# Kernel tuning notes

Measured on AMD Instinct MI355X. Metric: run time of the kernel, lower is better.

## Reference

```python
import jax, jax.numpy as jnp
import numpy as np

B, S, D = 2, 2048, 1024
H, K = 16, 64  # num_heads, n_hidden per head


def setup_inputs() -> dict:
    key = jax.random.key(0)
    ks = jax.random.split(key, 10)
    sc = 1.0 / np.sqrt(D)
    x = jax.random.normal(ks[0], (B, S, D), dtype=jnp.float32)
    attn_mask = jax.random.randint(ks[1], (B, S, S), 0, 2, dtype=jnp.int32)
    # per-head nn.Linear(d_input, n_hidden) weights stacked over heads: [H, D, K]
    W_Q = jax.random.normal(ks[2], (H, D, K), dtype=jnp.float32) * sc
    b_Q = jax.random.normal(ks[3], (H, K), dtype=jnp.float32) * sc
    W_K = jax.random.normal(ks[4], (H, D, K), dtype=jnp.float32) * sc
    b_K = jax.random.normal(ks[5], (H, K), dtype=jnp.float32) * sc
    W_V = jax.random.normal(ks[6], (H, D, K), dtype=jnp.float32) * sc
    b_V = jax.random.normal(ks[7], (H, K), dtype=jnp.float32) * sc
    # output projection nn.Linear(H*K, D)
    W_proj = jax.random.normal(ks[8], (H * K, D), dtype=jnp.float32) / np.sqrt(H * K)
    b_proj = jax.random.normal(ks[9], (D,), dtype=jnp.float32) / np.sqrt(H * K)
    return {"x": x, "W_Q": W_Q, "b_Q": b_Q, "W_K": W_K, "b_K": b_K,
            "W_V": W_V, "b_V": b_V, "W_proj": W_proj, "b_proj": b_proj,
            "attn_mask": attn_mask}


def reference(x, W_Q, b_Q, W_K, b_K, W_V, b_V, W_proj, b_proj, attn_mask):
    # Q/K/V for all heads at once: [B, H, S, K]
    Q = jnp.einsum('bsd,hdk->bhsk', x, W_Q) + b_Q[None, :, None, :]
    Kt = jnp.einsum('bsd,hdk->bhsk', x, W_K) + b_K[None, :, None, :]
    V = jnp.einsum('bsd,hdk->bhsk', x, W_V) + b_V[None, :, None, :]
    scale = 1.0 / np.sqrt(K).astype(np.float32)
    scores = jnp.einsum('bhsk,bhtk->bhst', Q, Kt) * scale  # [B,H,S,S]
    neg_inf = jnp.finfo(scores.dtype).min
    scores = jnp.where(attn_mask[:, None, :, :] == 0, neg_inf, scores)
    attn_scores = jax.nn.softmax(scores, axis=-1)  # [B,H,S,S]
    heads = jnp.einsum('bhst,bhtk->bhsk', attn_scores, V)  # [B,H,S,K]
    # concat heads along feature dim -> [B, S, H*K]
    concat = heads.transpose(0, 2, 1, 3).reshape(B, S, H * K)
    attn_output = concat @ W_proj + b_proj  # [B, S, D]
    return attn_output, attn_scores
```

## Files before the change

kernel.cpp:

```cpp
#include <hip/hip_runtime.h>

typedef unsigned short u16;
typedef unsigned long long u64;
typedef __attribute__((ext_vector_type(8))) short short8;
typedef __attribute__((ext_vector_type(8))) float float8;
typedef __attribute__((ext_vector_type(4))) float floatx4;

__device__ __forceinline__ float bf2f(u16 b) { return __uint_as_float(((unsigned)b) << 16); }
__device__ __forceinline__ u16 f2bf(float f) {
    unsigned u = __float_as_uint(f);
    return (u16)((u + 0x7FFFu + ((u >> 16) & 1u)) >> 16);
}

#define MFMA(a, b, c) __builtin_amdgcn_mfma_f32_16x16x32_bf16((a), (b), (c), 0, 0, 0)

#define AST 40
#define KST 72

__global__ __launch_bounds__(256) void k_proj_head(
    const float* __restrict__ x, const float* __restrict__ w, const float* __restrict__ bias,
    u16* __restrict__ out, int mode)
{
    int mt = blockIdx.x, h = blockIdx.y;
    int tid = threadIdx.x, wave = tid >> 6, lane = tid & 63;
    int col = lane & 15, quad = lane >> 4, m0 = wave * 16;
    int rg0 = mt * 64;

    __shared__ u16 As[64 * AST];
    __shared__ u16 Bs[64 * AST];

    floatx4 acc[4];
    for (int i = 0; i < 4; i++) acc[i] = (floatx4){0.f, 0.f, 0.f, 0.f};

    int lr = tid >> 2, lc = (tid & 3) * 8;
    int dr = tid >> 3, nc = (tid & 7) * 8;
    const float* wh = w + (size_t)h * 65536;

    for (int dk = 0; dk < 1024; dk += 32) {
        float8 av = *(const float8*)&x[(size_t)(rg0 + lr) * 1024 + dk + lc];
        short8 a8;
        #pragma unroll
        for (int j = 0; j < 8; j++) a8[j] = (short)f2bf(av[j]);
        *(short8*)&As[lr * AST + lc] = a8;
        float8 wv = *(const float8*)&wh[(size_t)(dk + dr) * 64 + nc];
        #pragma unroll
        for (int j = 0; j < 8; j++) Bs[(nc + j) * AST + dr] = f2bf(wv[j]);
        __syncthreads();
        short8 a = *(const short8*)&As[(m0 + col) * AST + quad * 8];
        #pragma unroll
        for (int nt = 0; nt < 4; nt++) {
            short8 b = *(const short8*)&Bs[(nt * 16 + col) * AST + quad * 8];
            acc[nt] = MFMA(a, b, acc[nt]);
        }
        __syncthreads();
    }
    #pragma unroll
    for (int nt = 0; nt < 4; nt++) {
        int n = nt * 16 + col;
        float bv = bias[h * 64 + n];
        #pragma unroll
        for (int r = 0; r < 4; r++) {
            int rowl = m0 + quad * 4 + r;
            int rg = rg0 + rowl;
            int bb = rg >> 11, s = rg & 2047;
            size_t bh = (size_t)(bb * 16 + h);
            float v = acc[nt][r] + bv;
            if (mode == 0) out[(bh * 2048 + s) * 64 + n] = f2bf(v);
            else           out[(bh * 64 + n) * 2048 + s] = f2bf(v);
        }
    }
}

__global__ __launch_bounds__(256) void k_pack(
    const int* __restrict__ mask, u64* __restrict__ bits)
{
    int row = blockIdx.x;
    int b = row >> 11, s = row & 2047;
    int wv = threadIdx.x >> 6, lane = threadIdx.x & 63;
    for (int w = wv; w < 32; w += 4) {
        int m = mask[(size_t)row * 2048 + w * 64 + lane];
        u64 bal = __ballot(m != 0);
        if (lane == 0) bits[((size_t)(b * 32 + w)) * 2048 + s] = bal;
    }
}

__global__ __launch_bounds__(256, 4) void k_fused(
    const float* __restrict__ x, const float* __restrict__ wq, const float* __restrict__ bq,
    const u16* __restrict__ Kbuf, const u16* __restrict__ Vt,
    const u64* __restrict__ mbits,
    float* __restrict__ sc, u16* __restrict__ concat)
{
    int st = blockIdx.x, bh = blockIdx.y;
    int b = bh >> 4, h = bh & 15;
    int s0 = st * 64;
    int tid = threadIdx.x, wave = tid >> 6, lane = tid & 63;
    int col = lane & 15, quad = lane >> 4, m0 = wave * 16;

    __shared__ __align__(16) char pool[3 * 64 * KST * 2];
    u16* Ks = (u16*)pool;
    u16* Vs = (u16*)(pool + 64 * KST * 2);
    u16* Ps = (u16*)(pool + 2 * 64 * KST * 2);
    u16* As = Ks;
    u16* Bs = Vs;
    u16* Qs = Ps;
    __shared__ u64 Mw[64];
    __shared__ float mrun[64], lrun[64];

    floatx4 acc[4];
    for (int i = 0; i < 4; i++) acc[i] = (floatx4){0.f, 0.f, 0.f, 0.f};
    int lr = tid >> 2, lc = (tid & 3) * 8;
    int dr = tid >> 3, nc = (tid & 7) * 8;
    const float* wh = wq + (size_t)h * 65536;
    const float* xb = x + ((size_t)b * 2048 + s0) * 1024;

    for (int dk = 0; dk < 1024; dk += 32) {
        float8 av = *(const float8*)&xb[(size_t)lr * 1024 + dk + lc];
        short8 a8;
        #pragma unroll
        for (int j = 0; j < 8; j++) a8[j] = (short)f2bf(av[j]);
        *(short8*)&As[lr * AST + lc] = a8;
        float8 wv = *(const float8*)&wh[(size_t)(dk + dr) * 64 + nc];
        #pragma unroll
        for (int j = 0; j < 8; j++) Bs[(nc + j) * AST + dr] = f2bf(wv[j]);
        __syncthreads();
        short8 a = *(const short8*)&As[(m0 + col) * AST + quad * 8];
        #pragma unroll
        for (int nt = 0; nt < 4; nt++) {
            short8 b2 = *(const short8*)&Bs[(nt * 16 + col) * AST + quad * 8];
            acc[nt] = MFMA(a, b2, acc[nt]);
        }
        __syncthreads();
    }
    if (tid < 64) { mrun[tid] = -1e30f; lrun[tid] = 0.f; }
    #pragma unroll
    for (int nt = 0; nt < 4; nt++) {
        int n = nt * 16 + col;
        float bv = bq[h * 64 + n];
        #pragma unroll
        for (int r = 0; r < 4; r++) {
            int rowl = m0 + quad * 4 + r;
            Qs[rowl * KST + n] = f2bf(acc[nt][r] + bv);
        }
    }
    __syncthreads();
    short8 aq0 = *(const short8*)&Qs[(m0 + col) * KST + quad * 8];
    short8 aq1 = *(const short8*)&Qs[(m0 + col) * KST + 32 + quad * 8];

    const u16* Kh = Kbuf + (size_t)bh * 2048 * 64;
    const u16* Vh = Vt + (size_t)bh * 64 * 2048;
    const u64* mrow = mbits + (size_t)b * 32 * 2048;
    int srow = tid >> 3, soff = (tid & 7) * 8;

    for (int t0 = 0; t0 < 2048; t0 += 64) {
        *(short8*)&Ks[srow * KST + soff]        = *(const short8*)&Kh[(size_t)(t0 + srow) * 64 + soff];
        *(short8*)&Ks[(srow + 32) * KST + soff] = *(const short8*)&Kh[(size_t)(t0 + srow + 32) * 64 + soff];
        if (tid < 64) Mw[tid] = mrow[(size_t)(t0 >> 6) * 2048 + s0 + tid];
        __syncthreads();
        floatx4 c4[4];
        #pragma unroll
        for (int nt = 0; nt < 4; nt++) {
            c4[nt] = (floatx4){0.f, 0.f, 0.f, 0.f};
            short8 b0 = *(const short8*)&Ks[(nt * 16 + col) * KST + quad * 8];
            short8 b1 = *(const short8*)&Ks[(nt * 16 + col) * KST + 32 + quad * 8];
            c4[nt] = MFMA(aq0, b0, c4[nt]);
            c4[nt] = MFMA(aq1, b1, c4[nt]);
        }
        #pragma unroll
        for (int r = 0; r < 4; r++) {
            int rowl = m0 + quad * 4 + r;
            u64 mw = Mw[rowl];
            float vv[4];
            float tm = -1e30f;
            #pragma unroll
            for (int nt = 0; nt < 4; nt++) {
                bool on = (mw >> (nt * 16 + col)) & 1ull;
                float v = on ? c4[nt][r] * 0.125f : -1e30f;
                vv[nt] = v;
                tm = fmaxf(tm, v);
            }
            tm = fmaxf(tm, __shfl_xor(tm, 1, 64));
            tm = fmaxf(tm, __shfl_xor(tm, 2, 64));
            tm = fmaxf(tm, __shfl_xor(tm, 4, 64));
            tm = fmaxf(tm, __shfl_xor(tm, 8, 64));
            float ts = 0.f;
            #pragma unroll
            for (int nt = 0; nt < 4; nt++)
                ts += (vv[nt] > -0.9e30f) ? __expf(vv[nt] - tm) : 0.f;
            ts += __shfl_xor(ts, 1, 64);
            ts += __shfl_xor(ts, 2, 64);
            ts += __shfl_xor(ts, 4, 64);
            ts += __shfl_xor(ts, 8, 64);
            if (col == 0 && tm > -0.9e30f) {
                float om = mrun[rowl];
                float nm = fmaxf(om, tm);
                lrun[rowl] = lrun[rowl] * __expf(om - nm) + ts * __expf(tm - nm);
                mrun[rowl] = nm;
            }
        }
        __syncthreads();
    }

    float mreg[4], rlreg[4];
    #pragma unroll
    for (int r = 0; r < 4; r++) {
        int rowl = m0 + quad * 4 + r;
        mreg[r] = mrun[rowl];
        float l = lrun[rowl];
        rlreg[r] = (l > 0.f) ? 1.0f / l : 0.f;
    }
    floatx4 accp[4];
    for (int i = 0; i < 4; i++) accp[i] = (floatx4){0.f, 0.f, 0.f, 0.f};
    float* scb = sc + (size_t)bh * 2048 * 2048;

    for (int t0 = 0; t0 < 2048; t0 += 64) {
        *(short8*)&Ks[srow * KST + soff]        = *(const short8*)&Kh[(size_t)(t0 + srow) * 64 + soff];
        *(short8*)&Ks[(srow + 32) * KST + soff] = *(const short8*)&Kh[(size_t)(t0 + srow + 32) * 64 + soff];
        *(short8*)&Vs[srow * KST + soff]        = *(const short8*)&Vh[(size_t)srow * 2048 + t0 + soff];
        *(short8*)&Vs[(srow + 32) * KST + soff] = *(const short8*)&Vh[(size_t)(srow + 32) * 2048 + t0 + soff];
        if (tid < 64) Mw[tid] = mrow[(size_t)(t0 >> 6) * 2048 + s0 + tid];
        __syncthreads();
        floatx4 c4[4];
        #pragma unroll
        for (int nt = 0; nt < 4; nt++) {
            c4[nt] = (floatx4){0.f, 0.f, 0.f, 0.f};
            short8 b0 = *(const short8*)&Ks[(nt * 16 + col) * KST + quad * 8];
            short8 b1 = *(const short8*)&Ks[(nt * 16 + col) * KST + 32 + quad * 8];
            c4[nt] = MFMA(aq0, b0, c4[nt]);
            c4[nt] = MFMA(aq1, b1, c4[nt]);
        }
        #pragma unroll
        for (int r = 0; r < 4; r++) {
            int rowl = m0 + quad * 4 + r;
            u64 mw = Mw[rowl];
            size_t base = (size_t)(s0 + rowl) * 2048 + t0;
            #pragma unroll
            for (int nt = 0; nt < 4; nt++) {
                bool on = (mw >> (nt * 16 + col)) & 1ull;
                float p = on ? __expf(c4[nt][r] * 0.125f - mreg[r]) * rlreg[r] : 0.f;
                scb[base + nt * 16 + col] = p;
                Ps[rowl * KST + nt * 16 + col] = f2bf(p);
            }
        }
        __syncthreads();
        short8 ap0 = *(const short8*)&Ps[(m0 + col) * KST + quad * 8];
        short8 ap1 = *(const short8*)&Ps[(m0 + col) * KST + 32 + quad * 8];
        #pragma unroll
        for (int nt = 0; nt < 4; nt++) {
            short8 b0 = *(const short8*)&Vs[(nt * 16 + col) * KST + quad * 8];
            short8 b1 = *(const short8*)&Vs[(nt * 16 + col) * KST + 32 + quad * 8];
            accp[nt] = MFMA(ap0, b0, accp[nt]);
            accp[nt] = MFMA(ap1, b1, accp[nt]);
        }
        __syncthreads();
    }
    #pragma unroll
    for (int nt = 0; nt < 4; nt++) {
        int n = nt * 16 + col;
        #pragma unroll
        for (int r = 0; r < 4; r++) {
            int rowl = m0 + quad * 4 + r;
            concat[((size_t)(b * 2048 + s0 + rowl)) * 1024 + h * 64 + n] = f2bf(accp[nt][r]);
        }
    }
}

__global__ __launch_bounds__(256) void k_out(
    const u16* __restrict__ concat, const float* __restrict__ wp,
    const float* __restrict__ bp, float* __restrict__ outp)
{
    int mt = blockIdx.x, ntile = blockIdx.y;
    int n0 = ntile * 64;
    int tid = threadIdx.x, wave = tid >> 6, lane = tid & 63;
    int col = lane & 15, quad = lane >> 4, m0 = wave * 16;
    int rg0 = mt * 64;

    __shared__ u16 As[64 * AST];
    __shared__ u16 Bs[64 * AST];

    floatx4 acc[4];
    for (int i = 0; i < 4; i++) acc[i] = (floatx4){0.f, 0.f, 0.f, 0.f};

    int lr = tid >> 2, lc = (tid & 3) * 8;
    int cr = tid >> 3, nc = (tid & 7) * 8;
    for (int c = 0; c < 1024; c += 32) {
        *(short8*)&As[lr * AST + lc] = *(const short8*)&concat[(size_t)(rg0 + lr) * 1024 + c + lc];
        float8 wv = *(const float8*)&wp[(size_t)(c + cr) * 1024 + n0 + nc];
        #pragma unroll
        for (int j = 0; j < 8; j++) Bs[(nc + j) * AST + cr] = f2bf(wv[j]);
        __syncthreads();
        short8 a = *(const short8*)&As[(m0 + col) * AST + quad * 8];
        #pragma unroll
        for (int nt = 0; nt < 4; nt++) {
            short8 b = *(const short8*)&Bs[(nt * 16 + col) * AST + quad * 8];
            acc[nt] = MFMA(a, b, acc[nt]);
        }
        __syncthreads();
    }
    #pragma unroll
    for (int nt = 0; nt < 4; nt++) {
        int n = n0 + nt * 16 + col;
        float bv = bp[n];
        #pragma unroll
        for (int r = 0; r < 4; r++) {
            int rowl = m0 + quad * 4 + r;
            outp[(size_t)(rg0 + rowl) * 1024 + n] = acc[nt][r] + bv;
        }
    }
}

extern "C" void kernel_launch(void* const* d_in, const int* in_sizes, int n_in,
                              void* d_out, int out_size, void* d_ws, size_t ws_size,
                              hipStream_t stream) {
    const float* x  = (const float*)d_in[0];
    const float* WQ = (const float*)d_in[1];
    const float* bQ = (const float*)d_in[2];
    const float* WK = (const float*)d_in[3];
    const float* bK = (const float*)d_in[4];
    const float* WV = (const float*)d_in[5];
    const float* bV = (const float*)d_in[6];
    const float* WP = (const float*)d_in[7];
    const float* bP = (const float*)d_in[8];
    const int* mask = (const int*)d_in[9];

    float* out = (float*)d_out;
    float* attn_out = out;
    float* sc = out + (size_t)4194304;

    const size_t NEED = (size_t)3 * 8388608 + 1048576;
    u16 *Kbuf, *Vtb, *concat;
    u64* mbits;
    if (ws_size >= NEED) {
        char* ws = (char*)d_ws;
        Kbuf   = (u16*)ws;               ws += 8388608;
        Vtb    = (u16*)ws;               ws += 8388608;
        concat = (u16*)ws;               ws += 8388608;
        mbits  = (u64*)ws;
    } else {
        Kbuf   = (u16*)attn_out;
        Vtb    = Kbuf + (size_t)4194304;
        mbits  = (u64*)d_in[3];
        concat = (u16*)d_in[9];
    }

    k_proj_head<<<dim3(64, 16), 256, 0, stream>>>(x, WK, bK, Kbuf, 0);
    k_proj_head<<<dim3(64, 16), 256, 0, stream>>>(x, WV, bV, Vtb, 1);
    k_pack<<<dim3(4096), 256, 0, stream>>>(mask, mbits);
    k_fused<<<dim3(32, 32), 256, 0, stream>>>(x, WQ, bQ, Kbuf, Vtb, mbits, sc, concat);
    k_out<<<dim3(64, 16), 256, 0, stream>>>(concat, WP, bP, attn_out);
}
```

Baseline: 961.9 us.

## Fuse K/V projections, prefetch global tiles into registers, transpose stats pass

Merges the K and V projection kernels into one that reads x once and writes transposed V through a shared-memory staging tile for coalesced stores. Adds register prefetch of the next global tile, overlapping loads with MFMA work, in the projection, fused attention and output kernels. Rewrites the softmax statistics pass to compute the transposed score tile, so each lane owns a query row and keeps running max and sum in registers with fewer shuffles and less shared-memory traffic. Prefetching raises register pressure and may lower occupancy.

```diff
diff --git a/kernel.cpp b/kernel.cpp
--- a/kernel.cpp
+++ b/kernel.cpp
@@ -6,7 +6,6 @@
 typedef __attribute__((ext_vector_type(8))) float float8;
 typedef __attribute__((ext_vector_type(4))) float floatx4;
 
-__device__ __forceinline__ float bf2f(u16 b) { return __uint_as_float(((unsigned)b) << 16); }
 __device__ __forceinline__ u16 f2bf(float f) {
     unsigned u = __float_as_uint(f);
     return (u16)((u + 0x7FFFu + ((u >> 16) & 1u)) >> 16);
@@ -17,57 +16,93 @@
 #define AST 40
 #define KST 72
 
-__global__ __launch_bounds__(256) void k_proj_head(
-    const float* __restrict__ x, const float* __restrict__ w, const float* __restrict__ bias,
-    u16* __restrict__ out, int mode)
+__global__ __launch_bounds__(256) void k_projkv(
+    const float* __restrict__ x,
+    const float* __restrict__ wk, const float* __restrict__ bk,
+    const float* __restrict__ wv, const float* __restrict__ bv,
+    u16* __restrict__ Kout, u16* __restrict__ Vout)
 {
     int mt = blockIdx.x, h = blockIdx.y;
     int tid = threadIdx.x, wave = tid >> 6, lane = tid & 63;
     int col = lane & 15, quad = lane >> 4, m0 = wave * 16;
     int rg0 = mt * 64;
 
-    __shared__ u16 As[64 * AST];
-    __shared__ u16 Bs[64 * AST];
-
-    floatx4 acc[4];
-    for (int i = 0; i < 4; i++) acc[i] = (floatx4){0.f, 0.f, 0.f, 0.f};
+    __shared__ __align__(16) char pool[3 * 64 * AST * 2];
+    u16* As = (u16*)pool;
+    u16* Bk = (u16*)(pool + 64 * AST * 2);
+    u16* Bv = (u16*)(pool + 2 * 64 * AST * 2);
+
+    floatx4 accK[4], accV[4];
+    for (int i = 0; i < 4; i++) { accK[i] = (floatx4){0,0,0,0}; accV[i] = (floatx4){0,0,0,0}; }
 
     int lr = tid >> 2, lc = (tid & 3) * 8;
     int dr = tid >> 3, nc = (tid & 7) * 8;
-    const float* wh = w + (size_t)h * 65536;
+    const float* whk = wk + (size_t)h * 65536;
+    const float* whv = wv + (size_t)h * 65536;
+
+    float8 av = *(const float8*)&x[(size_t)(rg0 + lr) * 1024 + lc];
+    float8 wkp = *(const float8*)&whk[(size_t)dr * 64 + nc];
+    float8 wvp = *(const float8*)&whv[(size_t)dr * 64 + nc];
 
     for (int dk = 0; dk < 1024; dk += 32) {
-        float8 av = *(const float8*)&x[(size_t)(rg0 + lr) * 1024 + dk + lc];
         short8 a8;
         #pragma unroll
         for (int j = 0; j < 8; j++) a8[j] = (short)f2bf(av[j]);
         *(short8*)&As[lr * AST + lc] = a8;
-        float8 wv = *(const float8*)&wh[(size_t)(dk + dr) * 64 + nc];
-        #pragma unroll
-        for (int j = 0; j < 8; j++) Bs[(nc + j) * AST + dr] = f2bf(wv[j]);
+        #pragma unroll
+        for (int j = 0; j < 8; j++) Bk[(nc + j) * AST + dr] = f2bf(wkp[j]);
+        #pragma unroll
+        for (int j = 0; j < 8; j++) Bv[(nc + j) * AST + dr] = f2bf(wvp[j]);
         __syncthreads();
+        if (dk + 32 < 1024) {
+            av  = *(const float8*)&x[(size_t)(rg0 + lr) * 1024 + dk + 32 + lc];
+            wkp = *(const float8*)&whk[(size_t)(dk + 32 + dr) * 64 + nc];
+            wvp = *(const float8*)&whv[(size_t)(dk + 32 + dr) * 64 + nc];
+        }
         short8 a = *(const short8*)&As[(m0 + col) * AST + quad * 8];
         #pragma unroll
         for (int nt = 0; nt < 4; nt++) {
-            short8 b = *(const short8*)&Bs[(nt * 16 + col) * AST + quad * 8];
-            acc[nt] = MFMA(a, b, acc[nt]);
+            short8 bkf = *(const short8*)&Bk[(nt * 16 + col) * AST + quad * 8];
+            short8 bvf = *(const short8*)&Bv[(nt * 16 + col) * AST + quad * 8];
+            accK[nt] = MFMA(a, bkf, accK[nt]);
+            accV[nt] = MFMA(a, bvf, accV[nt]);
         }
         __syncthreads();
     }
+
+    int bb = rg0 >> 11, s0 = rg0 & 2047;
+    size_t bh = (size_t)(bb * 16 + h);
+
     #pragma unroll
     for (int nt = 0; nt < 4; nt++) {
         int n = nt * 16 + col;
-        float bv = bias[h * 64 + n];
+        float bvl = bk[h * 64 + n];
         #pragma unroll
         for (int r = 0; r < 4; r++) {
             int rowl = m0 + quad * 4 + r;
-            int rg = rg0 + rowl;
-            int bb = rg >> 11, s = rg & 2047;
-            size_t bh = (size_t)(bb * 16 + h);
-            float v = acc[nt][r] + bv;
-            if (mode == 0) out[(bh * 2048 + s) * 64 + n] = f2bf(v);
-            else           out[(bh * 64 + n) * 2048 + s] = f2bf(v);
-        }
+            Kout[(bh * 2048 + s0 + rowl) * 64 + n] = f2bf(accK[nt][r] + bvl);
+        }
+    }
+
+    u16* VT = (u16*)pool;
+    #pragma unroll
+    for (int nt = 0; nt < 4; nt++) {
+        int n = nt * 16 + col;
+        float bvl = bv[h * 64 + n];
+        #pragma unroll
+        for (int r = 0; r < 4; r++) {
+            int rowl = m0 + quad * 4 + r;
+            VT[n * 68 + rowl] = f2bf(accV[nt][r] + bvl);
+        }
+    }
+    __syncthreads();
+    {
+        int n2 = tid >> 2, sseg = (tid & 3) * 16;
+        short8 p0 = *(const short8*)&VT[n2 * 68 + sseg];
+        short8 p1 = *(const short8*)&VT[n2 * 68 + sseg + 8];
+        u16* dst = &Vout[(bh * 64 + n2) * 2048 + s0 + sseg];
+        *(short8*)dst = p0;
+        *(short8*)(dst + 8) = p1;
     }
 }
 
@@ -107,39 +142,44 @@
     __shared__ float mrun[64], lrun[64];
 
     floatx4 acc[4];
-    for (int i = 0; i < 4; i++) acc[i] = (floatx4){0.f, 0.f, 0.f, 0.f};
+    for (int i = 0; i < 4; i++) acc[i] = (floatx4){0,0,0,0};
     int lr = tid >> 2, lc = (tid & 3) * 8;
     int dr = tid >> 3, nc = (tid & 7) * 8;
     const float* wh = wq + (size_t)h * 65536;
     const float* xb = x + ((size_t)b * 2048 + s0) * 1024;
 
-    for (int dk = 0; dk < 1024; dk += 32) {
-        float8 av = *(const float8*)&xb[(size_t)lr * 1024 + dk + lc];
-        short8 a8;
-        #pragma unroll
-        for (int j = 0; j < 8; j++) a8[j] = (short)f2bf(av[j]);
-        *(short8*)&As[lr * AST + lc] = a8;
-        float8 wv = *(const float8*)&wh[(size_t)(dk + dr) * 64 + nc];
-        #pragma unroll
-        for (int j = 0; j < 8; j++) Bs[(nc + j) * AST + dr] = f2bf(wv[j]);
-        __syncthreads();
-        short8 a = *(const short8*)&As[(m0 + col) * AST + quad * 8];
-        #pragma unroll
-        for (int nt = 0; nt < 4; nt++) {
-            short8 b2 = *(const short8*)&Bs[(nt * 16 + col) * AST + quad * 8];
-            acc[nt] = MFMA(a, b2, acc[nt]);
-        }
-        __syncthreads();
-    }
-    if (tid < 64) { mrun[tid] = -1e30f; lrun[tid] = 0.f; }
+    {
+        float8 av = *(const float8*)&xb[(size_t)lr * 1024 + lc];
+        float8 wv = *(const float8*)&wh[(size_t)dr * 64 + nc];
+        for (int dk = 0; dk < 1024; dk += 32) {
+            short8 a8;
+            #pragma unroll
+            for (int j = 0; j < 8; j++) a8[j] = (short)f2bf(av[j]);
+            *(short8*)&As[lr * AST + lc] = a8;
+            #pragma unroll
+            for (int j = 0; j < 8; j++) Bs[(nc + j) * AST + dr] = f2bf(wv[j]);
+            __syncthreads();
+            if (dk + 32 < 1024) {
+                av = *(const float8*)&xb[(size_t)lr * 1024 + dk + 32 + lc];
+                wv = *(const float8*)&wh[(size_t)(dk + 32 + dr) * 64 + nc];
+            }
+            short8 a = *(const short8*)&As[(m0 + col) * AST + quad * 8];
+            #pragma unroll
+            for (int nt = 0; nt < 4; nt++) {
+                short8 b2 = *(const short8*)&Bs[(nt * 16 + col) * AST + quad * 8];
+                acc[nt] = MFMA(a, b2, acc[nt]);
+            }
+            __syncthreads();
+        }
+    }
     #pragma unroll
     for (int nt = 0; nt < 4; nt++) {
         int n = nt * 16 + col;
-        float bv = bq[h * 64 + n];
+        float bvq = bq[h * 64 + n];
         #pragma unroll
         for (int r = 0; r < 4; r++) {
             int rowl = m0 + quad * 4 + r;
-            Qs[rowl * KST + n] = f2bf(acc[nt][r] + bv);
+            Qs[rowl * KST + n] = f2bf(acc[nt][r] + bvq);
         }
     }
     __syncthreads();
@@ -151,107 +191,125 @@
     const u64* mrow = mbits + (size_t)b * 32 * 2048;
     int srow = tid >> 3, soff = (tid & 7) * 8;
 
-    for (int t0 = 0; t0 < 2048; t0 += 64) {
-        *(short8*)&Ks[srow * KST + soff]        = *(const short8*)&Kh[(size_t)(t0 + srow) * 64 + soff];
-        *(short8*)&Ks[(srow + 32) * KST + soff] = *(const short8*)&Kh[(size_t)(t0 + srow + 32) * 64 + soff];
-        if (tid < 64) Mw[tid] = mrow[(size_t)(t0 >> 6) * 2048 + s0 + tid];
-        __syncthreads();
-        floatx4 c4[4];
-        #pragma unroll
-        for (int nt = 0; nt < 4; nt++) {
-            c4[nt] = (floatx4){0.f, 0.f, 0.f, 0.f};
-            short8 b0 = *(const short8*)&Ks[(nt * 16 + col) * KST + quad * 8];
-            short8 b1 = *(const short8*)&Ks[(nt * 16 + col) * KST + 32 + quad * 8];
-            c4[nt] = MFMA(aq0, b0, c4[nt]);
-            c4[nt] = MFMA(aq1, b1, c4[nt]);
-        }
-        #pragma unroll
-        for (int r = 0; r < 4; r++) {
-            int rowl = m0 + quad * 4 + r;
-            u64 mw = Mw[rowl];
-            float vv[4];
+    float mreg = -1e30f, lreg = 0.f;
+    {
+        short8 kp0 = *(const short8*)&Kh[(size_t)srow * 64 + soff];
+        short8 kp1 = *(const short8*)&Kh[(size_t)(srow + 32) * 64 + soff];
+        for (int t0 = 0; t0 < 2048; t0 += 64) {
+            *(short8*)&Ks[srow * KST + soff]        = kp0;
+            *(short8*)&Ks[(srow + 32) * KST + soff] = kp1;
+            if (tid < 64) Mw[tid] = mrow[(size_t)(t0 >> 6) * 2048 + s0 + tid];
+            __syncthreads();
+            if (t0 + 64 < 2048) {
+                kp0 = *(const short8*)&Kh[(size_t)(t0 + 64 + srow) * 64 + soff];
+                kp1 = *(const short8*)&Kh[(size_t)(t0 + 64 + srow + 32) * 64 + soff];
+            }
+            floatx4 c4[4];
+            #pragma unroll
+            for (int nt = 0; nt < 4; nt++) {
+                c4[nt] = (floatx4){0,0,0,0};
+                short8 b0 = *(const short8*)&Ks[(nt * 16 + col) * KST + quad * 8];
+                short8 b1 = *(const short8*)&Ks[(nt * 16 + col) * KST + 32 + quad * 8];
+                c4[nt] = MFMA(b0, aq0, c4[nt]);
+                c4[nt] = MFMA(b1, aq1, c4[nt]);
+            }
+            u64 mw = Mw[m0 + col];
             float tm = -1e30f;
             #pragma unroll
-            for (int nt = 0; nt < 4; nt++) {
-                bool on = (mw >> (nt * 16 + col)) & 1ull;
-                float v = on ? c4[nt][r] * 0.125f : -1e30f;
-                vv[nt] = v;
-                tm = fmaxf(tm, v);
-            }
-            tm = fmaxf(tm, __shfl_xor(tm, 1, 64));
-            tm = fmaxf(tm, __shfl_xor(tm, 2, 64));
-            tm = fmaxf(tm, __shfl_xor(tm, 4, 64));
-            tm = fmaxf(tm, __shfl_xor(tm, 8, 64));
+            for (int nt = 0; nt < 4; nt++)
+                #pragma unroll
+                for (int r = 0; r < 4; r++) {
+                    bool on = (mw >> (nt * 16 + quad * 4 + r)) & 1ull;
+                    float v = on ? c4[nt][r] * 0.125f : -1e30f;
+                    tm = fmaxf(tm, v);
+                }
+            tm = fmaxf(tm, __shfl_xor(tm, 16, 64));
+            tm = fmaxf(tm, __shfl_xor(tm, 32, 64));
             float ts = 0.f;
             #pragma unroll
             for (int nt = 0; nt < 4; nt++)
-                ts += (vv[nt] > -0.9e30f) ? __expf(vv[nt] - tm) : 0.f;
-            ts += __shfl_xor(ts, 1, 64);
-            ts += __shfl_xor(ts, 2, 64);
-            ts += __shfl_xor(ts, 4, 64);
-            ts += __shfl_xor(ts, 8, 64);
-            if (col == 0 && tm > -0.9e30f) {
-                float om = mrun[rowl];
-                float nm = fmaxf(om, tm);
-                lrun[rowl] = lrun[rowl] * __expf(om - nm) + ts * __expf(tm - nm);
-                mrun[rowl] = nm;
-            }
-        }
-        __syncthreads();
-    }
-
-    float mreg[4], rlreg[4];
+                #pragma unroll
+                for (int r = 0; r < 4; r++) {
+                    bool on = (mw >> (nt * 16 + quad * 4 + r)) & 1ull;
+                    ts += on ? __expf(c4[nt][r] * 0.125f - tm) : 0.f;
+                }
+            ts += __shfl_xor(ts, 16, 64);
+            ts += __shfl_xor(ts, 32, 64);
+            if (tm > -0.9e30f) {
+                float nm = fmaxf(mreg, tm);
+                lreg = lreg * __expf(mreg - nm) + ts * __expf(tm - nm);
+                mreg = nm;
+            }
+            __syncthreads();
+        }
+    }
+    if (quad == 0) { mrun[m0 + col] = mreg; lrun[m0 + col] = lreg; }
+    __syncthreads();
+
+    float mr4[4], rl4[4];
     #pragma unroll
     for (int r = 0; r < 4; r++) {
         int rowl = m0 + quad * 4 + r;
-        mreg[r] = mrun[rowl];
+        mr4[r] = mrun[rowl];
         float l = lrun[rowl];
-        rlreg[r] = (l > 0.f) ? 1.0f / l : 0.f;
+        rl4[r] = (l > 0.f) ? 1.0f / l : 0.f;
     }
     floatx4 accp[4];
-    for (int i = 0; i < 4; i++) accp[i] = (floatx4){0.f, 0.f, 0.f, 0.f};
+    for (int i = 0; i < 4; i++) accp[i] = (floatx4){0,0,0,0};
     float* scb = sc + (size_t)bh * 2048 * 2048;
 
-    for (int t0 = 0; t0 < 2048; t0 += 64) {
-        *(short8*)&Ks[srow * KST + soff]        = *(const short8*)&Kh[(size_t)(t0 + srow) * 64 + soff];
-        *(short8*)&Ks[(srow + 32) * KST + soff] = *(const short8*)&Kh[(size_t)(t0 + srow + 32) * 64 + soff];
-        *(short8*)&Vs[srow * KST + soff]        = *(const short8*)&Vh[(size_t)srow * 2048 + t0 + soff];
-        *(short8*)&Vs[(srow + 32) * KST + soff] = *(const short8*)&Vh[(size_t)(srow + 32) * 2048 + t0 + soff];
-        if (tid < 64) Mw[tid] = mrow[(size_t)(t0 >> 6) * 2048 + s0 + tid];
-        __syncthreads();
-        floatx4 c4[4];
-        #pragma unroll
-        for (int nt = 0; nt < 4; nt++) {
-            c4[nt] = (floatx4){0.f, 0.f, 0.f, 0.f};
-            short8 b0 = *(const short8*)&Ks[(nt * 16 + col) * KST + quad * 8];
-            short8 b1 = *(const short8*)&Ks[(nt * 16 + col) * KST + 32 + quad * 8];
-            c4[nt] = MFMA(aq0, b0, c4[nt]);
-            c4[nt] = MFMA(aq1, b1, c4[nt]);
-        }
-        #pragma unroll
-        for (int r = 0; r < 4; r++) {
-            int rowl = m0 + quad * 4 + r;
-            u64 mw = Mw[rowl];
-            size_t base = (size_t)(s0 + rowl) * 2048 + t0;
+    {
+        short8 kp0 = *(const short8*)&Kh[(size_t)srow * 64 + soff];
+        short8 kp1 = *(const short8*)&Kh[(size_t)(srow + 32) * 64 + soff];
+        short8 vp0 = *(const short8*)&Vh[(size_t)srow * 2048 + soff];
+        short8 vp1 = *(const short8*)&Vh[(size_t)(srow + 32) * 2048 + soff];
+        for (int t0 = 0; t0 < 2048; t0 += 64) {
+            *(short8*)&Ks[srow * KST + soff]        = kp0;
+            *(short8*)&Ks[(srow + 32) * KST + soff] = kp1;
+            *(short8*)&Vs[srow * KST + soff]        = vp0;
+            *(short8*)&Vs[(srow + 32) * KST + soff] = vp1;
+            if (tid < 64) Mw[tid] = mrow[(size_t)(t0 >> 6) * 2048 + s0 + tid];
+            __syncthreads();
+            if (t0 + 64 < 2048) {
+                kp0 = *(const short8*)&Kh[(size_t)(t0 + 64 + srow) * 64 + soff];
+                kp1 = *(const short8*)&Kh[(size_t)(t0 + 64 + srow + 32) * 64 + soff];
+                vp0 = *(const short8*)&Vh[(size_t)srow * 2048 + t0 + 64 + soff];
+                vp1 = *(const short8*)&Vh[(size_t)(srow + 32) * 2048 + t0 + 64 + soff];
+            }
+            floatx4 c4[4];
             #pragma unroll
             for (int nt = 0; nt < 4; nt++) {
-                bool on = (mw >> (nt * 16 + col)) & 1ull;
-                float p = on ? __expf(c4[nt][r] * 0.125f - mreg[r]) * rlreg[r] : 0.f;
-                scb[base + nt * 16 + col] = p;
-                Ps[rowl * KST + nt * 16 + col] = f2bf(p);
-            }
-        }
-        __syncthreads();
-        short8 ap0 = *(const short8*)&Ps[(m0 + col) * KST + quad * 8];
-        short8 ap1 = *(const short8*)&Ps[(m0 + col) * KST + 32 + quad * 8];
-        #pragma unroll
-        for (int nt = 0; nt < 4; nt++) {
-            short8 b0 = *(const short8*)&Vs[(nt * 16 + col) * KST + quad * 8];
-            short8 b1 = *(const short8*)&Vs[(nt * 16 + col) * KST + 32 + quad * 8];
-            accp[nt] = MFMA(ap0, b0, accp[nt]);
-            accp[nt] = MFMA(ap1, b1, accp[nt]);
-        }
-        __syncthreads();
+                c4[nt] = (floatx4){0,0,0,0};
+                short8 b0 = *(const short8*)&Ks[(nt * 16 + col) * KST + quad * 8];
+                short8 b1 = *(const short8*)&Ks[(nt * 16 + col) * KST + 32 + quad * 8];
+                c4[nt] = MFMA(aq0, b0, c4[nt]);
+                c4[nt] = MFMA(aq1, b1, c4[nt]);
+            }
+            #pragma unroll
+            for (int r = 0; r < 4; r++) {
+                int rowl = m0 + quad * 4 + r;
+                u64 mw = Mw[rowl];
+                size_t base = (size_t)(s0 + rowl) * 2048 + t0;
+                #pragma unroll
+                for (int nt = 0; nt < 4; nt++) {
+                    bool on = (mw >> (nt * 16 + col)) & 1ull;
+                    float p = on ? __expf(c4[nt][r] * 0.125f - mr4[r]) * rl4[r] : 0.f;
+                    scb[base + nt * 16 + col] = p;
+                    Ps[rowl * KST + nt * 16 + col] = f2bf(p);
+                }
+            }
+            __syncthreads();
+            short8 ap0 = *(const short8*)&Ps[(m0 + col) * KST + quad * 8];
+            short8 ap1 = *(const short8*)&Ps[(m0 + col) * KST + 32 + quad * 8];
+            #pragma unroll
+            for (int nt = 0; nt < 4; nt++) {
+                short8 b0 = *(const short8*)&Vs[(nt * 16 + col) * KST + quad * 8];
+                short8 b1 = *(const short8*)&Vs[(nt * 16 + col) * KST + 32 + quad * 8];
+                accp[nt] = MFMA(ap0, b0, accp[nt]);
+                accp[nt] = MFMA(ap1, b1, accp[nt]);
+            }
+            __syncthreads();
+        }
     }
     #pragma unroll
     for (int nt = 0; nt < 4; nt++) {
@@ -278,16 +336,21 @@
     __shared__ u16 Bs[64 * AST];
 
     floatx4 acc[4];
-    for (int i = 0; i < 4; i++) acc[i] = (floatx4){0.f, 0.f, 0.f, 0.f};
+    for (int i = 0; i < 4; i++) acc[i] = (floatx4){0,0,0,0};
 
     int lr = tid >> 2, lc = (tid & 3) * 8;
     int cr = tid >> 3, nc = (tid & 7) * 8;
+    short8 ap = *(const short8*)&concat[(size_t)(rg0 + lr) * 1024 + lc];
+    float8 wv = *(const float8*)&wp[(size_t)cr * 1024 + n0 + nc];
     for (int c = 0; c < 1024; c += 32) {
-        *(short8*)&As[lr * AST + lc] = *(const short8*)&concat[(size_t)(rg0 + lr) * 1024 + c + lc];
-        float8 wv = *(const float8*)&wp[(size_t)(c + cr) * 1024 + n0 + nc];
+        *(short8*)&As[lr * AST + lc] = ap;
         #pragma unroll
         for (int j = 0; j < 8; j++) Bs[(nc + j) * AST + cr] = f2bf(wv[j]);
         __syncthreads();
+        if (c + 32 < 1024) {
+            ap = *(const short8*)&concat[(size_t)(rg0 + lr) * 1024 + c + 32 + lc];
+            wv = *(const float8*)&wp[(size_t)(c + 32 + cr) * 1024 + n0 + nc];
+        }
         short8 a = *(const short8*)&As[(m0 + col) * AST + quad * 8];
         #pragma unroll
         for (int nt = 0; nt < 4; nt++) {
@@ -342,8 +405,7 @@
         concat = (u16*)d_in[9];
     }
 
-    k_proj_head<<<dim3(64, 16), 256, 0, stream>>>(x, WK, bK, Kbuf, 0);
-    k_proj_head<<<dim3(64, 16), 256, 0, stream>>>(x, WV, bV, Vtb, 1);
+    k_projkv<<<dim3(64, 16), 256, 0, stream>>>(x, WK, bK, WV, bV, Kbuf, Vtb);
     k_pack<<<dim3(4096), 256, 0, stream>>>(mask, mbits);
     k_fused<<<dim3(32, 32), 256, 0, stream>>>(x, WQ, bQ, Kbuf, Vtb, mbits, sc, concat);
     k_out<<<dim3(64, 16), 256, 0, stream>>>(concat, WP, bP, attn_out);
```

Result: faster. 853.8 us (-11.2%).
